# Kernel tuning notes

Hardware: AMD Instinct MI355X
Metric: run time of the kernel (lower is better)

Reference implementation:

```python
import jax, jax.numpy as jnp
import numpy as np

N = 50000      # nodes
E = 200000     # edges (before self-loops)
D_IN = 256
HID = 128
NEG_SLOPE = 0.2
BN_EPS = 1e-5


def _lin(k, fan_in, fan_out):
    return jax.random.normal(k, (fan_in, fan_out), jnp.float32) / np.float32(np.sqrt(fan_in))


def setup_inputs() -> dict:
    key = jax.random.key(0)
    ks = jax.random.split(key, 40)
    d = {}
    d['x'] = jax.random.normal(ks[0], (N, D_IN), jnp.float32)
    d['edge_index'] = jax.random.randint(ks[1], (2, E), 0, N, dtype=jnp.int32)
    # GAT layer 1: 256 -> 128, heads=4 (concat -> 512)
    d['W1'] = _lin(ks[2], D_IN, 4 * HID)
    d['asrc1'] = jax.random.normal(ks[3], (4, HID), jnp.float32) * 0.1
    d['adst1'] = jax.random.normal(ks[4], (4, HID), jnp.float32) * 0.1
    d['b1'] = jnp.zeros((4 * HID,), jnp.float32)
    d['g1'] = jax.random.uniform(ks[5], (4 * HID,), jnp.float32, 0.5, 1.5)
    d['be1'] = jax.random.normal(ks[6], (4 * HID,), jnp.float32) * 0.1
    d['m1'] = jax.random.normal(ks[7], (4 * HID,), jnp.float32) * 0.1
    d['v1'] = jax.random.uniform(ks[8], (4 * HID,), jnp.float32, 0.5, 1.5)
    # GAT layer 2: 512 -> 128, heads=4 (concat -> 512)
    d['W2'] = _lin(ks[9], 4 * HID, 4 * HID)
    d['asrc2'] = jax.random.normal(ks[10], (4, HID), jnp.float32) * 0.1
    d['adst2'] = jax.random.normal(ks[11], (4, HID), jnp.float32) * 0.1
    d['b2'] = jnp.zeros((4 * HID,), jnp.float32)
    d['g2'] = jax.random.uniform(ks[12], (4 * HID,), jnp.float32, 0.5, 1.5)
    d['be2'] = jax.random.normal(ks[13], (4 * HID,), jnp.float32) * 0.1
    d['m2'] = jax.random.normal(ks[14], (4 * HID,), jnp.float32) * 0.1
    d['v2'] = jax.random.uniform(ks[15], (4 * HID,), jnp.float32, 0.5, 1.5)
    # GAT layer 3: 512 -> 128, heads=1
    d['W3'] = _lin(ks[16], 4 * HID, HID)
    d['asrc3'] = jax.random.normal(ks[17], (1, HID), jnp.float32) * 0.1
    d['adst3'] = jax.random.normal(ks[18], (1, HID), jnp.float32) * 0.1
    d['b3'] = jnp.zeros((HID,), jnp.float32)
    d['g3'] = jax.random.uniform(ks[19], (HID,), jnp.float32, 0.5, 1.5)
    d['be3'] = jax.random.normal(ks[20], (HID,), jnp.float32) * 0.1
    d['m3'] = jax.random.normal(ks[21], (HID,), jnp.float32) * 0.1
    d['v3'] = jax.random.uniform(ks[22], (HID,), jnp.float32, 0.5, 1.5)
    # classifier head: 128 -> 64 -> 10
    d['Wc1'] = _lin(ks[23], HID, HID // 2)
    d['bc1'] = jnp.zeros((HID // 2,), jnp.float32)
    d['Wc2'] = _lin(ks[24], HID // 2, 10)
    d['bc2'] = jnp.zeros((10,), jnp.float32)
    return d


def _gat_layer(h, src, dst, W, asrc, adst, b, heads, ch):
    # PyG GATConv (eval mode): linear -> per-head scores -> segment softmax over dst -> aggregate
    xp = (h @ W).reshape(-1, heads, ch)                 # [N, H, C]
    e_src = (xp * asrc[None]).sum(-1)                   # [N, H]
    e_dst = (xp * adst[None]).sum(-1)                   # [N, H]
    e = jax.nn.leaky_relu(e_src[src] + e_dst[dst], NEG_SLOPE)  # [E', H]
    m = jax.lax.stop_gradient(jax.ops.segment_max(e, dst, num_segments=N))
    w = jnp.exp(e - m[dst])
    s = jax.ops.segment_sum(w, dst, num_segments=N)     # [N, H]
    alpha = w / (s[dst] + 1e-16)                        # [E', H]
    out = jax.ops.segment_sum(alpha[:, :, None] * xp[src], dst, num_segments=N)  # [N, H, C]
    return out.reshape(-1, heads * ch) + b


def _bn_relu(h, g, be, mu, var):
    return jax.nn.relu((h - mu) * jax.lax.rsqrt(var + BN_EPS) * g + be)


def reference(x, edge_index,
              W1, asrc1, adst1, b1, g1, be1, m1, v1,
              W2, asrc2, adst2, b2, g2, be2, m2, v2,
              W3, asrc3, adst3, b3, g3, be3, m3, v3,
              Wc1, bc1, Wc2, bc2):
    loop = jnp.arange(N, dtype=edge_index.dtype)
    src = jnp.concatenate([edge_index[0], loop])        # GATConv adds self-loops
    dst = jnp.concatenate([edge_index[1], loop])
    h = _bn_relu(_gat_layer(x, src, dst, W1, asrc1, adst1, b1, 4, HID), g1, be1, m1, v1)
    h = _bn_relu(_gat_layer(h, src, dst, W2, asrc2, adst2, b2, 4, HID), g2, be2, m2, v2)
    h = _bn_relu(_gat_layer(h, src, dst, W3, asrc3, adst3, b3, 1, HID), g3, be3, m3, v3)
    E_GNN = h                                           # [N, 128]
    logits = jax.nn.relu(E_GNN @ Wc1 + bc1) @ Wc2 + bc2 # [N, 10]
    P_GNN = jax.nn.softmax(logits, axis=-1)
    return (E_GNN, P_GNN)
```

## Files before the change

### kernel.cpp

```cpp
#include <hip/hip_runtime.h>
#include <math.h>

#define N_NODES 50000
#define N_EDGES 200000
#define NEG_SLOPE 0.2f
#define BN_EPS 1e-5f

#define SCAN_ELEMS 1024
#define SCAN_NB ((N_NODES + SCAN_ELEMS - 1) / SCAN_ELEMS)

typedef __attribute__((ext_vector_type(4))) float f32x4;
typedef __attribute__((ext_vector_type(8))) short bf16x8;
typedef __attribute__((ext_vector_type(8))) ushort u16x8;
typedef __attribute__((ext_vector_type(2))) ushort u16x2;

__device__ __forceinline__ ushort f2bf(float x) {
    unsigned u = __float_as_uint(x);
    u += 0x7FFFu + ((u >> 16) & 1u);
    return (ushort)(u >> 16);
}
__device__ __forceinline__ float bf2f(ushort u) {
    return __uint_as_float(((unsigned)u) << 16);
}

__global__ void k_init(int* cnt, int* off) {
    int i = blockIdx.x * blockDim.x + threadIdx.x;
    if (i < N_NODES) { cnt[i] = 1; off[i] = 1; }
}

__global__ void k_count(const int* __restrict__ ei, int* cnt) {
    int e = blockIdx.x * blockDim.x + threadIdx.x;
    if (e < N_EDGES) atomicAdd(&cnt[ei[N_EDGES + e]], 1);
}

__global__ __launch_bounds__(256) void k_scan1(const int* __restrict__ cnt,
                                               int* __restrict__ incl,
                                               int* __restrict__ partials) {
    __shared__ int sh[256];
    const int t = threadIdx.x;
    const int base = blockIdx.x * SCAN_ELEMS + t * 4;
    int v0 = 0, v1 = 0, v2 = 0, v3 = 0;
    if (base + 3 < N_NODES) {
        int4 lv = *reinterpret_cast<const int4*>(&cnt[base]);
        v0 = lv.x; v1 = lv.y; v2 = lv.z; v3 = lv.w;
    } else {
        if (base + 0 < N_NODES) v0 = cnt[base + 0];
        if (base + 1 < N_NODES) v1 = cnt[base + 1];
        if (base + 2 < N_NODES) v2 = cnt[base + 2];
        if (base + 3 < N_NODES) v3 = cnt[base + 3];
    }
    const int s1 = v0 + v1, s2 = s1 + v2, s3 = s2 + v3;
    sh[t] = s3;
    __syncthreads();
#pragma unroll
    for (int off = 1; off < 256; off <<= 1) {
        int x = (t >= off) ? sh[t - off] : 0;
        __syncthreads();
        sh[t] += x;
        __syncthreads();
    }
    const int excl = sh[t] - s3;
    if (base + 0 < N_NODES) incl[base + 0] = excl + v0;
    if (base + 1 < N_NODES) incl[base + 1] = excl + s1;
    if (base + 2 < N_NODES) incl[base + 2] = excl + s2;
    if (base + 3 < N_NODES) incl[base + 3] = excl + s3;
    if (t == 255) partials[blockIdx.x] = sh[255];
}

__global__ void k_scan2(const int* __restrict__ partials, int* __restrict__ pofs) {
    if (threadIdx.x == 0) {
        int s = 0;
        for (int b = 0; b < SCAN_NB; ++b) { pofs[b] = s; s += partials[b]; }
    }
}

__global__ void k_scan3(const int* __restrict__ incl, const int* __restrict__ pofs,
                        int* __restrict__ row_ptr) {
    int i = blockIdx.x * blockDim.x + threadIdx.x;
    if (i < N_NODES) row_ptr[i + 1] = incl[i] + pofs[i >> 10];
    if (i == 0) row_ptr[0] = 0;
}

__global__ void k_self(const int* __restrict__ row_ptr, int* colb) {
    int n = blockIdx.x * blockDim.x + threadIdx.x;
    if (n < N_NODES) colb[row_ptr[n]] = n;
}

__global__ void k_scatter(const int* __restrict__ ei, const int* __restrict__ row_ptr,
                          int* off, int* colb) {
    int e = blockIdx.x * blockDim.x + threadIdx.x;
    if (e < N_EDGES) {
        int dst = ei[N_EDGES + e];
        int p = atomicAdd(&off[dst], 1);
        colb[row_ptr[dst] + p] = ei[e];
    }
}

__global__ void k_cvt(const float* __restrict__ in, ushort* __restrict__ out, int n4) {
    int i = blockIdx.x * blockDim.x + threadIdx.x;
    if (i < n4) {
        float4 v = reinterpret_cast<const float4*>(in)[i];
        ushort4 o;
        o.x = f2bf(v.x); o.y = f2bf(v.y); o.z = f2bf(v.z); o.w = f2bf(v.w);
        reinterpret_cast<ushort4*>(out)[i] = o;
    }
}

__global__ void k_wt(const float* __restrict__ W, ushort* __restrict__ Wt, int K, int N) {
    int idx = blockIdx.x * blockDim.x + threadIdx.x;
    if (idx < K * N) {
        int n = idx / K, k = idx - n * K;
        Wt[idx] = f2bf(W[(size_t)k * N + n]);
    }
}

__global__ __launch_bounds__(256) void k_gemm_bf16(const ushort* __restrict__ A,
                                                   const ushort* __restrict__ Bt,
                                                   ushort* __restrict__ Cb,
                                                   const float* __restrict__ asrc,
                                                   const float* __restrict__ adst,
                                                   float* __restrict__ es,
                                                   float* __restrict__ ed,
                                                   int M, int K, int N) {
    __shared__ __align__(16) ushort As[128 * 32];
    __shared__ __align__(16) ushort Bs[128 * 32];
    __shared__ float sles[2][128];
    __shared__ float sled[2][128];
    const int tid = threadIdx.x;
    const int wid = tid >> 6, lane = tid & 63;
    const int wm = wid >> 1, wn = wid & 1;
    const int row0 = blockIdx.x * 128, col0 = blockIdx.y * 128;
    const int H = N >> 7;

    const int c0 = wid * 2;
    const int sub = lane >> 2;
    const int kcol = (lane & 3) * 8;

    int ar0 = row0 + c0 * 16 + sub;      if (ar0 > M - 1) ar0 = M - 1;
    int ar1 = row0 + c0 * 16 + 16 + sub; if (ar1 > M - 1) ar1 = M - 1;
    const size_t gA0 = (size_t)ar0 * K + kcol;
    const size_t gA1 = (size_t)ar1 * K + kcol;
    const size_t gB0 = (size_t)(col0 + c0 * 16 + sub) * K + kcol;
    const size_t gB1 = gB0 + (size_t)16 * K;
    ushort* lA0 = As + c0 * 512;
    ushort* lA1 = lA0 + 512;
    ushort* lB0 = Bs + c0 * 512;
    ushort* lB1 = lB0 + 512;

    const int afr = (wm * 64 + (lane & 15)) * 32 + (lane >> 4) * 8;
    const int bfr = (wn * 64 + (lane & 15)) * 32 + (lane >> 4) * 8;

    f32x4 acc[4][4] = {};

    for (int k0 = 0; k0 < K; k0 += 32) {
        __builtin_amdgcn_global_load_lds(
            (const __attribute__((address_space(1))) unsigned*)(A + gA0 + k0),
            (__attribute__((address_space(3))) unsigned*)lA0, 16, 0, 0);
        __builtin_amdgcn_global_load_lds(
            (const __attribute__((address_space(1))) unsigned*)(A + gA1 + k0),
            (__attribute__((address_space(3))) unsigned*)lA1, 16, 0, 0);
        __builtin_amdgcn_global_load_lds(
            (const __attribute__((address_space(1))) unsigned*)(Bt + gB0 + k0),
            (__attribute__((address_space(3))) unsigned*)lB0, 16, 0, 0);
        __builtin_amdgcn_global_load_lds(
            (const __attribute__((address_space(1))) unsigned*)(Bt + gB1 + k0),
            (__attribute__((address_space(3))) unsigned*)lB1, 16, 0, 0);
        __syncthreads();

        bf16x8 af[4], bg[4];
#pragma unroll
        for (int m = 0; m < 4; ++m)
            af[m] = *reinterpret_cast<const bf16x8*>(&As[afr + m * 16 * 32]);
#pragma unroll
        for (int n = 0; n < 4; ++n)
            bg[n] = *reinterpret_cast<const bf16x8*>(&Bs[bfr + n * 16 * 32]);
#pragma unroll
        for (int m = 0; m < 4; ++m)
#pragma unroll
            for (int n = 0; n < 4; ++n)
                acc[m][n] = __builtin_amdgcn_mfma_f32_16x16x32_bf16(af[m], bg[n], acc[m][n], 0, 0, 0);
        __syncthreads();
    }

    const int crow = row0 + wm * 64 + (lane >> 4) * 4;
    const int ccol = col0 + wn * 64 + (lane & 15);
#pragma unroll
    for (int m = 0; m < 4; ++m) {
#pragma unroll
        for (int j = 0; j < 4; ++j) {
            int r = crow + m * 16 + j;
            if (r < M) {
#pragma unroll
                for (int n = 0; n < 4; ++n)
                    Cb[(size_t)r * N + ccol + n * 16] = f2bf(acc[m][n][j]);
            }
        }
    }

    float as_c[4], ad_c[4];
#pragma unroll
    for (int n = 0; n < 4; ++n) {
        int cl = wn * 64 + n * 16 + (lane & 15);
        as_c[n] = asrc[blockIdx.y * 128 + cl];
        ad_c[n] = adst[blockIdx.y * 128 + cl];
    }
#pragma unroll
    for (int m = 0; m < 4; ++m) {
#pragma unroll
        for (int j = 0; j < 4; ++j) {
            float ps = acc[m][0][j] * as_c[0] + acc[m][1][j] * as_c[1] +
                       acc[m][2][j] * as_c[2] + acc[m][3][j] * as_c[3];
            float pd = acc[m][0][j] * ad_c[0] + acc[m][1][j] * ad_c[1] +
                       acc[m][2][j] * ad_c[2] + acc[m][3][j] * ad_c[3];
#pragma unroll
            for (int o = 1; o < 16; o <<= 1) {
                ps += __shfl_xor(ps, o);
                pd += __shfl_xor(pd, o);
            }
            if ((lane & 15) == 0) {
                int rl = wm * 64 + (lane >> 4) * 4 + m * 16 + j;
                sles[wn][rl] = ps;
                sled[wn][rl] = pd;
            }
        }
    }
    __syncthreads();
    if (tid < 128) {
        int r = row0 + tid;
        if (r < M) {
            es[(size_t)r * H + blockIdx.y] = sles[0][tid] + sles[1][tid];
            ed[(size_t)r * H + blockIdx.y] = sled[0][tid] + sled[1][tid];
        }
    }
}

template <int H, bool BF16OUT>
__global__ __launch_bounds__(64) void k_agg(
    const ushort* __restrict__ xpb, const float* __restrict__ es, const float* __restrict__ ed,
    const int* __restrict__ row_ptr, const int* __restrict__ colb,
    const float* __restrict__ bias, const float* __restrict__ gg, const float* __restrict__ be,
    const float* __restrict__ mu, const float* __restrict__ var, void* __restrict__ outv) {
    constexpr int HC = H * 128;
    constexpr int CPT = HC / 64;
    constexpr int CHUNK = 128;
    constexpr int GS = (H == 4) ? 16 : 64;
    __shared__ int s_src[CHUNK];
    __shared__ float s_w[CHUNK][H];
    const int n = blockIdx.x;
    const int lane = threadIdx.x;
    const int g = (H == 4) ? (lane >> 4) : 0;
    const int gl = (H == 4) ? (lane & 15) : lane;
    const int beg = row_ptr[n], end = row_ptr[n + 1];
    const int cnt = end - beg;

    float edn[H];
#pragma unroll
    for (int h = 0; h < H; ++h) edn[h] = ed[n * H + h];

    float acc[CPT];
#pragma unroll
    for (int j = 0; j < CPT; ++j) acc[j] = 0.f;
    float m_run = -INFINITY, s_run = 0.f;
    const int ch0 = lane * CPT;
    const ushort* xb = xpb + ch0;

    for (int cbeg = 0; cbeg < cnt; cbeg += CHUNK) {
        const int cc = min(cnt - cbeg, CHUNK);
        for (int i = lane; i < cc; i += 64) {
            int src = colb[beg + cbeg + i];
            s_src[i] = src;
            if (H == 4) {
                float4 e4 = *reinterpret_cast<const float4*>(&es[src * 4]);
                float4 o;
                o.x = e4.x + edn[0]; o.x = (o.x > 0.f) ? o.x : NEG_SLOPE * o.x;
                o.y = e4.y + edn[1]; o.y = (o.y > 0.f) ? o.y : NEG_SLOPE * o.y;
                o.z = e4.z + edn[2]; o.z = (o.z > 0.f) ? o.z : NEG_SLOPE * o.z;
                o.w = e4.w + edn[3]; o.w = (o.w > 0.f) ? o.w : NEG_SLOPE * o.w;
                *reinterpret_cast<float4*>(&s_w[i][0]) = o;
            } else {
                float e = es[src] + edn[0];
                s_w[i][0] = (e > 0.f) ? e : NEG_SLOPE * e;
            }
        }
        __syncthreads();
        float cm = -INFINITY;
        for (int i = gl; i < cc; i += GS) cm = fmaxf(cm, s_w[i][g]);
#pragma unroll
        for (int o = GS >> 1; o; o >>= 1) cm = fmaxf(cm, __shfl_xor(cm, o));
        const float m_new = fmaxf(m_run, cm);
        const float scale = __expf(m_run - m_new);
        float sl = 0.f;
        for (int i = gl; i < cc; i += GS) {
            float w = __expf(s_w[i][g] - m_new);
            s_w[i][g] = w;
            sl += w;
        }
#pragma unroll
        for (int o = GS >> 1; o; o >>= 1) sl += __shfl_xor(sl, o);
        s_run = s_run * scale + sl;
        m_run = m_new;
#pragma unroll
        for (int j = 0; j < CPT; ++j) acc[j] *= scale;
        __syncthreads();
        for (int e = 0; e < cc; e += 4) {
            float w0 = s_w[e][g];
            int   p0 = s_src[e];
            float w1 = 0.f; int p1 = n;
            float w2 = 0.f; int p2 = n;
            float w3 = 0.f; int p3 = n;
            if (e + 1 < cc) { w1 = s_w[e + 1][g]; p1 = s_src[e + 1]; }
            if (e + 2 < cc) { w2 = s_w[e + 2][g]; p2 = s_src[e + 2]; }
            if (e + 3 < cc) { w3 = s_w[e + 3][g]; p3 = s_src[e + 3]; }
            if (CPT == 8) {
                u16x8 v0 = *reinterpret_cast<const u16x8*>(xb + (size_t)p0 * HC);
                u16x8 v1 = *reinterpret_cast<const u16x8*>(xb + (size_t)p1 * HC);
                u16x8 v2 = *reinterpret_cast<const u16x8*>(xb + (size_t)p2 * HC);
                u16x8 v3 = *reinterpret_cast<const u16x8*>(xb + (size_t)p3 * HC);
#pragma unroll
                for (int j = 0; j < CPT; ++j) {
                    float a = acc[j];
                    a = fmaf(w0, bf2f(v0[j]), a);
                    a = fmaf(w1, bf2f(v1[j]), a);
                    a = fmaf(w2, bf2f(v2[j]), a);
                    a = fmaf(w3, bf2f(v3[j]), a);
                    acc[j] = a;
                }
            } else {
                u16x2 v0 = *reinterpret_cast<const u16x2*>(xb + (size_t)p0 * HC);
                u16x2 v1 = *reinterpret_cast<const u16x2*>(xb + (size_t)p1 * HC);
                u16x2 v2 = *reinterpret_cast<const u16x2*>(xb + (size_t)p2 * HC);
                u16x2 v3 = *reinterpret_cast<const u16x2*>(xb + (size_t)p3 * HC);
#pragma unroll
                for (int j = 0; j < CPT; ++j) {
                    float a = acc[j];
                    a = fmaf(w0, bf2f(v0[j]), a);
                    a = fmaf(w1, bf2f(v1[j]), a);
                    a = fmaf(w2, bf2f(v2[j]), a);
                    a = fmaf(w3, bf2f(v3[j]), a);
                    acc[j] = a;
                }
            }
        }
        __syncthreads();
    }

    const float inv = 1.f / (s_run + 1e-16f);
    float vals[CPT];
#pragma unroll
    for (int j = 0; j < CPT; ++j) {
        int ch = ch0 + j;
        float val = acc[j] * inv + bias[ch];
        val = (val - mu[ch]) * (gg[ch] * rsqrtf(var[ch] + BN_EPS)) + be[ch];
        vals[j] = fmaxf(val, 0.f);
    }
    if (BF16OUT) {
        if (CPT == 8) {
            u16x8 o;
#pragma unroll
            for (int j = 0; j < CPT; ++j) o[j] = f2bf(vals[j]);
            *reinterpret_cast<u16x8*>((ushort*)outv + (size_t)n * HC + ch0) = o;
        } else {
            u16x2 o;
#pragma unroll
            for (int j = 0; j < CPT; ++j) o[j] = f2bf(vals[j]);
            *reinterpret_cast<u16x2*>((ushort*)outv + (size_t)n * HC + ch0) = o;
        }
    } else {
        float2 o = make_float2(vals[0], vals[1 % CPT]);
        *reinterpret_cast<float2*>((float*)outv + (size_t)n * HC + ch0) = o;
    }
}

#define CLS_NB 16
__global__ __launch_bounds__(256) void k_cls(const float* __restrict__ Eg,
                                             const float* __restrict__ Wc1,
                                             const float* __restrict__ bc1,
                                             const float* __restrict__ Wc2,
                                             const float* __restrict__ bc2,
                                             float* __restrict__ P) {
    __shared__ float Ws[128 * 64];
    __shared__ float W2s[64 * 10 + 16];
    __shared__ float b1s[64];
    __shared__ float e_sh[CLS_NB][128];
    __shared__ float h_sh[CLS_NB][64];
    __shared__ float l_sh[CLS_NB][10];
    const int t = threadIdx.x;
    const int n0 = blockIdx.x * CLS_NB;

    for (int i = t; i < 2048; i += 256)
        reinterpret_cast<float4*>(Ws)[i] = reinterpret_cast<const float4*>(Wc1)[i];
    for (int i = t; i < 640; i += 256) W2s[i] = Wc2[i];
    if (t < 64) b1s[t] = bc1[t];
    if (t >= 64 && t < 74) W2s[640 + t - 64] = bc2[t - 64];
    for (int i = t; i < CLS_NB * 32; i += 256) {
        int node = i >> 5, q = i & 31;
        reinterpret_cast<float4*>(&e_sh[node][0])[q] =
            reinterpret_cast<const float4*>(&Eg[(size_t)(n0 + node) * 128])[q];
    }
    __syncthreads();

    {
        const int c = t & 63, ng = t >> 6;
        float acc0 = b1s[c], acc1 = b1s[c], acc2 = b1s[c], acc3 = b1s[c];
        for (int k = 0; k < 128; ++k) {
            float w = Ws[k * 64 + c];
            acc0 = fmaf(e_sh[ng * 4 + 0][k], w, acc0);
            acc1 = fmaf(e_sh[ng * 4 + 1][k], w, acc1);
            acc2 = fmaf(e_sh[ng * 4 + 2][k], w, acc2);
            acc3 = fmaf(e_sh[ng * 4 + 3][k], w, acc3);
        }
        h_sh[ng * 4 + 0][c] = fmaxf(acc0, 0.f);
        h_sh[ng * 4 + 1][c] = fmaxf(acc1, 0.f);
        h_sh[ng * 4 + 2][c] = fmaxf(acc2, 0.f);
        h_sh[ng * 4 + 3][c] = fmaxf(acc3, 0.f);
    }
    __syncthreads();
    if (t < CLS_NB * 10) {
        int node = t / 10, c = t - node * 10;
        float acc = W2s[640 + c];
        for (int k = 0; k < 64; ++k) acc = fmaf(h_sh[node][k], W2s[k * 10 + c], acc);
        l_sh[node][c] = acc;
    }
    __syncthreads();
    if (t < CLS_NB) {
        float mx = l_sh[t][0];
        for (int j = 1; j < 10; ++j) mx = fmaxf(mx, l_sh[t][j]);
        float s = 0.f;
        float ex[10];
        for (int j = 0; j < 10; ++j) { ex[j] = __expf(l_sh[t][j] - mx); s += ex[j]; }
        float inv = 1.f / s;
        for (int j = 0; j < 10; ++j) l_sh[t][j] = ex[j] * inv;
    }
    __syncthreads();
    if (t < CLS_NB * 10) {
        int node = t / 10, c = t - node * 10;
        P[(size_t)(n0 + node) * 10 + c] = l_sh[node][c];
    }
}

extern "C" void kernel_launch(void* const* d_in, const int* in_sizes, int n_in,
                              void* d_out, int out_size, void* d_ws, size_t ws_size,
                              hipStream_t stream) {
    const float* x     = (const float*)d_in[0];
    const int*   ei    = (const int*)d_in[1];
    const float* W1    = (const float*)d_in[2];
    const float* asrc1 = (const float*)d_in[3];
    const float* adst1 = (const float*)d_in[4];
    const float* b1    = (const float*)d_in[5];
    const float* gg1   = (const float*)d_in[6];
    const float* be1   = (const float*)d_in[7];
    const float* mu1   = (const float*)d_in[8];
    const float* v1    = (const float*)d_in[9];
    const float* W2    = (const float*)d_in[10];
    const float* asrc2 = (const float*)d_in[11];
    const float* adst2 = (const float*)d_in[12];
    const float* b2    = (const float*)d_in[13];
    const float* gg2   = (const float*)d_in[14];
    const float* be2   = (const float*)d_in[15];
    const float* mu2   = (const float*)d_in[16];
    const float* v2    = (const float*)d_in[17];
    const float* W3    = (const float*)d_in[18];
    const float* asrc3 = (const float*)d_in[19];
    const float* adst3 = (const float*)d_in[20];
    const float* b3    = (const float*)d_in[21];
    const float* gg3   = (const float*)d_in[22];
    const float* be3   = (const float*)d_in[23];
    const float* mu3   = (const float*)d_in[24];
    const float* v3    = (const float*)d_in[25];
    const float* Wc1   = (const float*)d_in[26];
    const float* bc1   = (const float*)d_in[27];
    const float* Wc2   = (const float*)d_in[28];
    const float* bc2   = (const float*)d_in[29];

    ushort* xpb  = (ushort*)d_ws;
    ushort* hh   = xpb + (size_t)N_NODES * 512;
    ushort* wt1  = hh + (size_t)N_NODES * 512;
    ushort* wt2  = wt1 + 512 * 256;
    ushort* wt3  = wt2 + 512 * 512;
    float*  es   = (float*)(wt3 + 128 * 512);
    float*  ed   = es + (size_t)N_NODES * 4;
    int* cnt     = (int*)(ed + (size_t)N_NODES * 4);
    int* off     = cnt + N_NODES;
    int* row_ptr = off + N_NODES;
    int* colb    = row_ptr + N_NODES + 4;
    int* incl    = colb + N_EDGES + N_NODES;
    int* partials = incl + N_NODES;
    int* pofs    = partials + SCAN_NB;

    float* Egnn = (float*)d_out;
    float* P    = Egnn + (size_t)N_NODES * 128;

    k_init<<<(N_NODES + 255) / 256, 256, 0, stream>>>(cnt, off);
    k_count<<<(N_EDGES + 255) / 256, 256, 0, stream>>>(ei, cnt);
    k_scan1<<<SCAN_NB, 256, 0, stream>>>(cnt, incl, partials);
    k_scan2<<<1, 64, 0, stream>>>(partials, pofs);
    k_scan3<<<(N_NODES + 255) / 256, 256, 0, stream>>>(incl, pofs, row_ptr);
    k_self<<<(N_NODES + 255) / 256, 256, 0, stream>>>(row_ptr, colb);
    k_scatter<<<(N_EDGES + 255) / 256, 256, 0, stream>>>(ei, row_ptr, off, colb);

    k_wt<<<(512 * 256 + 255) / 256, 256, 0, stream>>>(W1, wt1, 256, 512);
    k_wt<<<(512 * 512 + 255) / 256, 256, 0, stream>>>(W2, wt2, 512, 512);
    k_wt<<<(128 * 512 + 255) / 256, 256, 0, stream>>>(W3, wt3, 512, 128);
    {
        int n4 = N_NODES * 256 / 4;
        k_cvt<<<(n4 + 255) / 256, 256, 0, stream>>>(x, hh, n4);
    }

    const int mt = (N_NODES + 127) / 128;

    {
        dim3 grid(mt, 4);
        k_gemm_bf16<<<grid, 256, 0, stream>>>(hh, wt1, xpb, asrc1, adst1, es, ed,
                                              N_NODES, 256, 512);
    }
    k_agg<4, true><<<N_NODES, 64, 0, stream>>>(xpb, es, ed, row_ptr, colb,
                                               b1, gg1, be1, mu1, v1, hh);
    {
        dim3 grid(mt, 4);
        k_gemm_bf16<<<grid, 256, 0, stream>>>(hh, wt2, xpb, asrc2, adst2, es, ed,
                                              N_NODES, 512, 512);
    }
    k_agg<4, true><<<N_NODES, 64, 0, stream>>>(xpb, es, ed, row_ptr, colb,
                                               b2, gg2, be2, mu2, v2, hh);
    {
        dim3 grid(mt, 1);
        k_gemm_bf16<<<grid, 256, 0, stream>>>(hh, wt3, xpb, asrc3, adst3, es, ed,
                                              N_NODES, 512, 128);
    }
    k_agg<1, false><<<N_NODES, 64, 0, stream>>>(xpb, es, ed, row_ptr, colb,
                                                b3, gg3, be3, mu3, v3, Egnn);
    k_cls<<<(N_NODES + CLS_NB - 1) / CLS_NB, 256, 0, stream>>>(Egnn, Wc1, bc1, Wc2, bc2, P);
}
```

Baseline: 467.5 us.

## Use 128x256 GEMM tiles with XCD-aware block remapping for 512-wide layers

New measurement: 524.8 us. +12.2%, slower.

```diff
diff --git a/kernel.cpp b/kernel.cpp
--- a/kernel.cpp
+++ b/kernel.cpp
@@ -111,6 +111,127 @@
     if (idx < K * N) {
         int n = idx / K, k = idx - n * K;
         Wt[idx] = f2bf(W[(size_t)k * N + n]);
+    }
+}
+
+__global__ __launch_bounds__(256) void k_gemm256(const ushort* __restrict__ A,
+                                                 const ushort* __restrict__ Bt,
+                                                 ushort* __restrict__ Cb,
+                                                 const float* __restrict__ asrc,
+                                                 const float* __restrict__ adst,
+                                                 float* __restrict__ es,
+                                                 float* __restrict__ ed,
+                                                 int M, int K) {
+    constexpr int N = 512;
+    __shared__ __align__(16) ushort As[128 * 32];
+    __shared__ __align__(16) ushort Bs[256 * 32];
+    const int tid = threadIdx.x;
+    const int wid = tid >> 6, lane = tid & 63;
+    const int wm = wid >> 1, wn = wid & 1;
+
+    const int nwg = gridDim.x;
+    const int q = nwg >> 3, r = nwg & 7;
+    const int xcd = blockIdx.x & 7, bidx = blockIdx.x >> 3;
+    const int wg = ((xcd < r) ? xcd * (q + 1) : r * (q + 1) + (xcd - r) * q) + bidx;
+    const int row0 = (wg >> 1) * 128;
+    const int by = wg & 1;
+    const int col0 = by * 256;
+    const int head = by * 2 + wn;
+
+    const int sub = lane >> 2;
+    const int kcol = (lane & 3) * 8;
+
+    const ushort* gPtr[6];
+    ushort* lBase[6];
+#pragma unroll
+    for (int c = 0; c < 6; ++c) {
+        int chunk = wid * 6 + c;
+        if (chunk < 8) {
+            int ar = row0 + chunk * 16 + sub;
+            if (ar > M - 1) ar = M - 1;
+            gPtr[c] = A + (size_t)ar * K + kcol;
+            lBase[c] = As + chunk * 512;
+        } else {
+            int bc = chunk - 8;
+            gPtr[c] = Bt + (size_t)(col0 + bc * 16 + sub) * K + kcol;
+            lBase[c] = Bs + bc * 512;
+        }
+    }
+
+    const int afr = (wm * 64 + (lane & 15)) * 32 + (lane >> 4) * 8;
+    const int bfr0 = (wn * 128 + (lane & 15)) * 32 + (lane >> 4) * 8;
+
+    f32x4 acc[4][8] = {};
+
+    for (int k0 = 0; k0 < K; k0 += 32) {
+#pragma unroll
+        for (int c = 0; c < 6; ++c) {
+            __builtin_amdgcn_global_load_lds(
+                (const __attribute__((address_space(1))) unsigned*)(gPtr[c] + k0),
+                (__attribute__((address_space(3))) unsigned*)lBase[c], 16, 0, 0);
+        }
+        __syncthreads();
+
+        bf16x8 af[4], bg[8];
+#pragma unroll
+        for (int m = 0; m < 4; ++m)
+            af[m] = *reinterpret_cast<const bf16x8*>(&As[afr + m * 16 * 32]);
+#pragma unroll
+        for (int n = 0; n < 8; ++n)
+            bg[n] = *reinterpret_cast<const bf16x8*>(&Bs[bfr0 + n * 16 * 32]);
+#pragma unroll
+        for (int m = 0; m < 4; ++m)
+#pragma unroll
+            for (int n = 0; n < 8; ++n)
+                acc[m][n] = __builtin_amdgcn_mfma_f32_16x16x32_bf16(af[m], bg[n], acc[m][n], 0, 0, 0);
+        __syncthreads();
+    }
+
+    const int crow = row0 + wm * 64 + (lane >> 4) * 4;
+    const int ccol = col0 + wn * 128 + (lane & 15);
+#pragma unroll
+    for (int m = 0; m < 4; ++m) {
+#pragma unroll
+        for (int j = 0; j < 4; ++j) {
+            int rr = crow + m * 16 + j;
+            if (rr < M) {
+#pragma unroll
+                for (int n = 0; n < 8; ++n)
+                    Cb[(size_t)rr * N + ccol + n * 16] = f2bf(acc[m][n][j]);
+            }
+        }
+    }
+
+    float as_c[8], ad_c[8];
+#pragma unroll
+    for (int n = 0; n < 8; ++n) {
+        int cl = n * 16 + (lane & 15);
+        as_c[n] = asrc[head * 128 + cl];
+        ad_c[n] = adst[head * 128 + cl];
+    }
+#pragma unroll
+    for (int m = 0; m < 4; ++m) {
+#pragma unroll
+        for (int j = 0; j < 4; ++j) {
+            float ps = 0.f, pd = 0.f;
+#pragma unroll
+            for (int n = 0; n < 8; ++n) {
+                ps = fmaf(acc[m][n][j], as_c[n], ps);
+                pd = fmaf(acc[m][n][j], ad_c[n], pd);
+            }
+#pragma unroll
+            for (int o = 1; o < 16; o <<= 1) {
+                ps += __shfl_xor(ps, o);
+                pd += __shfl_xor(pd, o);
+            }
+            if ((lane & 15) == 0) {
+                int rr = crow + m * 16 + j;
+                if (rr < M) {
+                    es[(size_t)rr * 4 + head] = ps;
+                    ed[(size_t)rr * 4 + head] = pd;
+                }
+            }
+        }
     }
 }
 
@@ -507,19 +628,14 @@
     }
 
     const int mt = (N_NODES + 127) / 128;
-
-    {
-        dim3 grid(mt, 4);
-        k_gemm_bf16<<<grid, 256, 0, stream>>>(hh, wt1, xpb, asrc1, adst1, es, ed,
-                                              N_NODES, 256, 512);
-    }
+    const int nwg256 = mt * 2;
+
+    k_gemm256<<<nwg256, 256, 0, stream>>>(hh, wt1, xpb, asrc1, adst1, es, ed,
+                                          N_NODES, 256);
     k_agg<4, true><<<N_NODES, 64, 0, stream>>>(xpb, es, ed, row_ptr, colb,
                                                b1, gg1, be1, mu1, v1, hh);
-    {
-        dim3 grid(mt, 4);
-        k_gemm_bf16<<<grid, 256, 0, stream>>>(hh, wt2, xpb, asrc2, adst2, es, ed,
-                                              N_NODES, 512, 512);
-    }
+    k_gemm256<<<nwg256, 256, 0, stream>>>(hh, wt2, xpb, asrc2, adst2, es, ed,
+                                          N_NODES, 512);
     k_agg<4, true><<<N_NODES, 64, 0, stream>>>(xpb, es, ed, row_ptr, colb,
                                                b2, gg2, be2, mu2, v2, hh);
     {
```
